# Optimization experiments

Measured on AMD Instinct MI355X. Metric: run time of the kernel, lower is better.

The kernel has to match this reference:

```python
import jax, jax.numpy as jnp
import numpy as np


def setup_inputs() -> dict:
    key = jax.random.key(0)
    k1, k2 = jax.random.split(key)
    B, T = 16, 2048
    n_fft = 1024
    hop_length = 256
    win_length = 1024
    N = n_fft // 2 + 1  # 513 rfft bins
    spec_real = jax.random.normal(k1, (B, N, T), dtype=jnp.float32)
    spec_imag = jax.random.normal(k2, (B, N, T), dtype=jnp.float32)
    # periodic Hann window (torch.hann_window default)
    n = jnp.arange(win_length, dtype=jnp.float32)
    window = 0.5 * (1.0 - jnp.cos(2.0 * jnp.pi * n / win_length))
    return {
        "spec_real": spec_real,
        "spec_imag": spec_imag,
        "window": window,
        "n_fft": n_fft,
        "hop_length": hop_length,
        "win_length": win_length,
    }


def reference(spec_real, spec_imag, window, n_fft, hop_length, win_length):
    pad = (win_length - hop_length) // 2
    B, N, T = spec_real.shape
    spec = spec_real + 1j * spec_imag  # [B, N, T] complex
    # irfft along freq dim with 'backward' norm (jnp default): [B, n_fft, T]
    ifft = jnp.fft.irfft(spec, n=n_fft, axis=1)
    ifft = ifft * window[None, :, None]  # windowed frames
    L = (T - 1) * hop_length + win_length  # overlap-add output length
    # scatter indices: sample positions of each frame, shape [win_length, T]
    idx = jnp.arange(T)[None, :] * hop_length + jnp.arange(win_length)[:, None]
    y = jnp.zeros((B, L), dtype=ifft.dtype).at[:, idx].add(ifft)
    y = y[:, pad:L - pad]
    # window-squared envelope, same overlap-add pattern
    wsq = jnp.broadcast_to((window * window)[:, None], (win_length, T))
    env = jnp.zeros((L,), dtype=window.dtype).at[idx].add(wsq)[pad:L - pad]
    return y / env
```

## Files before the change

kernel.cpp:

```cpp
#include <hip/hip_runtime.h>

#define BB 16
#define TT 2048
#define NROW 513
#define HOP 256
#define OUTLB 524288
#define FTO 28
#define SPAN (FTO*HOP)
#define TILES 74
#define RZ 513

__device__ __forceinline__ int brev9(int k){ return (int)(__brev((unsigned)k)>>23); }
__device__ __forceinline__ int zidx(int f,int m){ return f*RZ + (m ^ ((m>>4)&28) ^ (f<<2)); }

__global__ __launch_bounds__(512,2) void istft_fused(
    const float* __restrict__ sr, const float* __restrict__ si,
    const float* __restrict__ win, float* __restrict__ out)
{
  __shared__ float2 zc[8*RZ];
  __shared__ __align__(16) float2 ola[SPAN/2];
  __shared__ float2 ttab[256];
  __shared__ float2 wtab[512];

  const int tid  = threadIdx.x;
  const int b    = blockIdx.x / TILES;
  const int tile = blockIdx.x % TILES;
  const int L0   = tile*SPAN + 384;
  const int Tbase= tile*FTO - 2;

  if (tid < 256) {
    float s,c; __sincosf((float)tid*0.012271846303085130f,&s,&c);
    ttab[tid]=make_float2(c,s);
  }
  {
    float2 wv = ((const float2*)win)[tid];
    wtab[tid] = make_float2(wv.x*(1.f/512.f), wv.y*(1.f/512.f));
  }
  for (int i=tid;i<SPAN/2;i+=512) ola[i]=make_float2(0.f,0.f);

  const int f  = tid & 7;
  const int pp = tid >> 3;
  const float* srb = sr + (size_t)b*NROW*TT;
  const float* sib = si + (size_t)b*NROW*TT;

  float ctw[4], stw[4];
  #pragma unroll
  for (int cc=0;cc<4;++cc){
    __sincosf((float)(cc*64+pp)*0.006135923151542565f,&stw[cc],&ctw[cc]);
  }

  auto storeZ = [&](int cc, float ar,float ai,float br,float bi,float cr,float ci){
    int k = cc*64+pp;
    if (k==0){
      zc[zidx(f,0)] = make_float2(0.5f*(ar+br), 0.5f*(ar-br));
      zc[zidx(f,1)] = make_float2(cr, -ci);
    } else {
      float Er=0.5f*(ar+br), Ei=0.5f*(ai-bi);
      float Dr=0.5f*(ar-br), Di=0.5f*(ai+bi);
      float Or=Dr*ctw[cc]-Di*stw[cc], Oi=Dr*stw[cc]+Di*ctw[cc];
      zc[zidx(f,brev9(k))]     = make_float2(Er-Oi, Ei+Or);
      zc[zidx(f,brev9(512-k))] = make_float2(Er+Oi, Or-Ei);
    }
  };

  auto do_fft = [&](){
    #pragma unroll
    for (int st=0; st<4; ++st){
      __syncthreads();
      const int h = 1<<(2*st);
      #pragma unroll
      for (int i=0;i<2;++i){
        int q   = pp + 64*i;
        int ilo = q & (h-1);
        int base= ((q>>(2*st))<<(2*st+2)) + ilo;
        float2 w1 = ttab[ilo<<(8-2*st)];
        float2 w2 = ttab[ilo<<(7-2*st)];
        float2 e0=zc[zidx(f,base)],     e1=zc[zidx(f,base+h)];
        float2 e2=zc[zidx(f,base+2*h)], e3=zc[zidx(f,base+3*h)];
        float t1r=e1.x*w1.x-e1.y*w1.y, t1i=e1.x*w1.y+e1.y*w1.x;
        float t3r=e3.x*w1.x-e3.y*w1.y, t3i=e3.x*w1.y+e3.y*w1.x;
        float arr=e0.x+t1r, ari=e0.y+t1i, brr=e0.x-t1r, bri=e0.y-t1i;
        float crr=e2.x+t3r, cri=e2.y+t3i, drr=e2.x-t3r, dri=e2.y-t3i;
        float cwr=crr*w2.x-cri*w2.y, cwi=crr*w2.y+cri*w2.x;
        float dwr=drr*w2.x-dri*w2.y, dwi=drr*w2.y+dri*w2.x;
        zc[zidx(f,base)]     = make_float2(arr+cwr, ari+cwi);
        zc[zidx(f,base+2*h)] = make_float2(arr-cwr, ari-cwi);
        zc[zidx(f,base+h)]   = make_float2(brr-dwi, bri+dwr);
        zc[zidx(f,base+3*h)] = make_float2(brr+dwi, bri-dwr);
      }
    }
    __syncthreads();
    #pragma unroll
    for (int i=0;i<4;++i){
      int q = pp + 64*i;
      float2 tw = ttab[q];
      float2 u = zc[zidx(f,q)], v = zc[zidx(f,q+256)];
      float tr=v.x*tw.x-v.y*tw.y, ti=v.x*tw.y+v.y*tw.x;
      zc[zidx(f,q)]     = make_float2(u.x+tr, u.y+ti);
      zc[zidx(f,q+256)] = make_float2(u.x-tr, u.y-ti);
    }
  };

  auto do_ola = [&](int chunkT){
    #pragma unroll
    for (int g=0; g<4; ++g){
      __syncthreads();
      int slot = g + 4*(tid>>8);
      int tg   = chunkT + slot;
      int offB = tg*HOP - L0;
      bool vt  = (tg>=0 && tg<TT);
      int mbq  = tid & 255;
      #pragma unroll
      for (int i=0;i<2;++i){
        int m = mbq + 256*i;
        float2 v = zc[zidx(slot,m)];
        float2 w = wtab[m];
        int idx = offB + 2*m;
        if (vt && idx>=0 && idx<SPAN){
          float2 o = ola[idx>>1];
          o.x += v.x*w.x;
          o.y += v.y*w.y;
          ola[idx>>1] = o;
        }
      }
    }
  };

  for (int half=0; half<2; ++half){
    const int c0  = 2*half;
    const int ta  = Tbase + 8*c0 + f;
    const int tb_ = ta + 8;
    const int tca = min(max(ta ,0),TT-1);
    const int tcb = min(max(tb_,0),TT-1);
    const float ma  = (ta >=0 && ta <TT)?1.f:0.f;
    const float mb2 = (tb_>=0 && tb_<TT)?1.f:0.f;

    float sAr[4],sAi[4],sBr[4],sBi[4];
    float sCr=0.f, sCi=0.f;

    __syncthreads();
    #pragma unroll
    for (int cc=0;cc<4;++cc){
      int k = cc*64+pp;
      const float* pr  = srb + (size_t)k*TT;
      const float* pi_ = sib + (size_t)k*TT;
      const float* qr  = srb + (size_t)(512-k)*TT;
      const float* qi  = sib + (size_t)(512-k)*TT;
      float ar0=pr [tca], ar1=pr [tcb];
      float ai0=pi_[tca], ai1=pi_[tcb];
      float br0=qr [tca], br1=qr [tcb];
      float bi0=qi [tca], bi1=qi [tcb];
      sAr[cc]=ar1; sAi[cc]=ai1; sBr[cc]=br1; sBi[cc]=bi1;
      float cr0=0.f, ci0=0.f;
      if (cc==0 && pp==0){
        const float* rr = srb + (size_t)256*TT;
        const float* ri = sib + (size_t)256*TT;
        cr0 = rr[tca]; sCr = rr[tcb];
        ci0 = ri[tca]; sCi = ri[tcb];
      }
      storeZ(cc, ar0*ma, ai0*ma, br0*ma, bi0*ma, cr0*ma, ci0*ma);
    }
    do_fft();
    do_ola(Tbase + 8*c0);

    __syncthreads();
    #pragma unroll
    for (int cc=0;cc<4;++cc){
      storeZ(cc, sAr[cc]*mb2, sAi[cc]*mb2, sBr[cc]*mb2, sBi[cc]*mb2, sCr*mb2, sCi*mb2);
    }
    do_fft();
    do_ola(Tbase + 8*(c0+1));
  }
  __syncthreads();

  const bool edge = (tile==0)|(tile==TILES-1);
  float* outb = out + (size_t)b*OUTLB;
  #pragma unroll
  for (int i=0;i<4;++i){
    int i4 = tid + 512*i;
    if (i4 < SPAN/4){
      int s  = 4*i4;
      int gs = tile*SPAN + s;
      if (gs < OUTLB){
        float4 v = ((const float4*)ola)[i4];
        float r[4]={v.x,v.y,v.z,v.w};
        if (!edge){
          #pragma unroll
          for(int e=0;e<4;++e) r[e] *= (2.f/3.f);
        } else {
          #pragma unroll
          for(int e=0;e<4;++e){
            int l = L0 + s + e;
            int j0 = l & 255, tb = l >> 8;
            float env=0.f;
            #pragma unroll
            for (int mm=0;mm<4;++mm){
              int t2 = tb-mm;
              if (t2>=0 && t2<TT){
                float wv = 0.5f-0.5f*__cosf((float)(j0+256*mm)*0.006135923151542565f);
                env += wv*wv;
              }
            }
            r[e] /= env;
          }
        }
        *(float4*)(outb+gs) = make_float4(r[0],r[1],r[2],r[3]);
      }
    }
  }
}

extern "C" void kernel_launch(void* const* d_in, const int* in_sizes, int n_in,
                              void* d_out, int out_size, void* d_ws, size_t ws_size,
                              hipStream_t stream) {
  const float* sr = (const float*)d_in[0];
  const float* si = (const float*)d_in[1];
  const float* w  = (const float*)d_in[2];
  float* out = (float*)d_out;
  istft_fused<<<BB*TILES, 512, 0, stream>>>(sr, si, w, out);
}
```

Baseline: 253.0 us.

## Replace shared-memory overlap-add scatter with register-held gather accumulation

Removes the shared OLA buffer and instead has each thread own fixed output sample pairs, gathering windowed IFFT contributions from all frames in the chunk into register accumulators. This eliminates the four syncthreads-separated scatter phases per chunk and the read-modify-write traffic to shared memory, and frees LDS so more blocks can be resident (launch bounds raised to 4). The 1/512 normalization moves into the input masks. Costs are seven float2 accumulators per thread and possible register pressure at the higher occupancy target, plus variable-trip inner loops.

New measurement: 248.0 us. -2.0%, faster.

```diff
diff --git a/kernel.cpp b/kernel.cpp
--- a/kernel.cpp
+++ b/kernel.cpp
@@ -13,30 +13,28 @@
 __device__ __forceinline__ int brev9(int k){ return (int)(__brev((unsigned)k)>>23); }
 __device__ __forceinline__ int zidx(int f,int m){ return f*RZ + (m ^ ((m>>4)&28) ^ (f<<2)); }
 
-__global__ __launch_bounds__(512,2) void istft_fused(
+__global__ __launch_bounds__(512,4) void istft_fused(
     const float* __restrict__ sr, const float* __restrict__ si,
     const float* __restrict__ win, float* __restrict__ out)
 {
   __shared__ float2 zc[8*RZ];
-  __shared__ __align__(16) float2 ola[SPAN/2];
   __shared__ float2 ttab[256];
   __shared__ float2 wtab[512];
 
   const int tid  = threadIdx.x;
   const int b    = blockIdx.x / TILES;
   const int tile = blockIdx.x % TILES;
-  const int L0   = tile*SPAN + 384;
   const int Tbase= tile*FTO - 2;
 
-  if (tid < 256) {
+  if (tid < 256){
     float s,c; __sincosf((float)tid*0.012271846303085130f,&s,&c);
     ttab[tid]=make_float2(c,s);
   }
-  {
-    float2 wv = ((const float2*)win)[tid];
-    wtab[tid] = make_float2(wv.x*(1.f/512.f), wv.y*(1.f/512.f));
-  }
-  for (int i=tid;i<SPAN/2;i+=512) ola[i]=make_float2(0.f,0.f);
+  wtab[tid] = ((const float2*)win)[tid];
+
+  float2 acc[7];
+  #pragma unroll
+  for (int i=0;i<7;++i) acc[i]=make_float2(0.f,0.f);
 
   const int f  = tid & 7;
   const int pp = tid >> 3;
@@ -101,27 +99,20 @@
     }
   };
 
-  auto do_ola = [&](int chunkT){
-    #pragma unroll
-    for (int g=0; g<4; ++g){
-      __syncthreads();
-      int slot = g + 4*(tid>>8);
-      int tg   = chunkT + slot;
-      int offB = tg*HOP - L0;
-      bool vt  = (tg>=0 && tg<TT);
-      int mbq  = tid & 255;
-      #pragma unroll
-      for (int i=0;i<2;++i){
-        int m = mbq + 256*i;
-        float2 v = zc[zidx(slot,m)];
-        float2 w = wtab[m];
-        int idx = offB + 2*m;
-        if (vt && idx>=0 && idx<SPAN){
-          float2 o = ola[idx>>1];
-          o.x += v.x*w.x;
-          o.y += v.y*w.y;
-          ola[idx>>1] = o;
-        }
+  auto do_gather = [&](int c){
+    __syncthreads();
+    const int jb = 896 - 2048*c;
+    #pragma unroll
+    for (int i=0;i<7;++i){
+      int j0 = 2*(tid + 512*i) + jb;
+      int s_lo = max(0, (j0-768)>>8);
+      int s_hi = min(7, j0>>8);
+      for (int s=s_lo; s<=s_hi; ++s){
+        int m0 = (j0 - 256*s)>>1;
+        float2 v = zc[zidx(s,m0)];
+        float2 w = wtab[m0];
+        acc[i].x += v.x*w.x;
+        acc[i].y += v.y*w.y;
       }
     }
   };
@@ -132,8 +123,8 @@
     const int tb_ = ta + 8;
     const int tca = min(max(ta ,0),TT-1);
     const int tcb = min(max(tb_,0),TT-1);
-    const float ma  = (ta >=0 && ta <TT)?1.f:0.f;
-    const float mb2 = (tb_>=0 && tb_<TT)?1.f:0.f;
+    const float ma  = (ta >=0 && ta <TT)?(1.f/512.f):0.f;
+    const float mb2 = (tb_>=0 && tb_<TT)?(1.f/512.f):0.f;
 
     float sAr[4],sAi[4],sBr[4],sBi[4];
     float sCr=0.f, sCi=0.f;
@@ -161,7 +152,7 @@
       storeZ(cc, ar0*ma, ai0*ma, br0*ma, bi0*ma, cr0*ma, ci0*ma);
     }
     do_fft();
-    do_ola(Tbase + 8*c0);
+    do_gather(c0);
 
     __syncthreads();
     #pragma unroll
@@ -169,43 +160,38 @@
       storeZ(cc, sAr[cc]*mb2, sAi[cc]*mb2, sBr[cc]*mb2, sBi[cc]*mb2, sCr*mb2, sCi*mb2);
     }
     do_fft();
-    do_ola(Tbase + 8*(c0+1));
-  }
-  __syncthreads();
+    do_gather(c0+1);
+  }
 
   const bool edge = (tile==0)|(tile==TILES-1);
   float* outb = out + (size_t)b*OUTLB;
+  const int gbase = tile*SPAN;
   #pragma unroll
-  for (int i=0;i<4;++i){
-    int i4 = tid + 512*i;
-    if (i4 < SPAN/4){
-      int s  = 4*i4;
-      int gs = tile*SPAN + s;
-      if (gs < OUTLB){
-        float4 v = ((const float4*)ola)[i4];
-        float r[4]={v.x,v.y,v.z,v.w};
-        if (!edge){
+  for (int i=0;i<7;++i){
+    int p0 = 2*(tid + 512*i);
+    int gs = gbase + p0;
+    if (gs < OUTLB){
+      float2 r = acc[i];
+      if (!edge){
+        r.x *= (2.f/3.f); r.y *= (2.f/3.f);
+      } else {
+        #pragma unroll
+        for (int e=0;e<2;++e){
+          int l = gbase + 384 + p0 + e;
+          int j0 = l & 255, tb = l >> 8;
+          float env=0.f;
           #pragma unroll
-          for(int e=0;e<4;++e) r[e] *= (2.f/3.f);
-        } else {
-          #pragma unroll
-          for(int e=0;e<4;++e){
-            int l = L0 + s + e;
-            int j0 = l & 255, tb = l >> 8;
-            float env=0.f;
-            #pragma unroll
-            for (int mm=0;mm<4;++mm){
-              int t2 = tb-mm;
-              if (t2>=0 && t2<TT){
-                float wv = 0.5f-0.5f*__cosf((float)(j0+256*mm)*0.006135923151542565f);
-                env += wv*wv;
-              }
+          for (int mm=0;mm<4;++mm){
+            int t2 = tb-mm;
+            if (t2>=0 && t2<TT){
+              float wv = 0.5f-0.5f*__cosf((float)(j0+256*mm)*0.006135923151542565f);
+              env += wv*wv;
             }
-            r[e] /= env;
           }
+          ((float*)&r)[e] /= env;
         }
-        *(float4*)(outb+gs) = make_float4(r[0],r[1],r[2],r[3]);
-      }
+      }
+      *(float2*)(outb+gs) = r;
     }
   }
 }
```
